# Performance work log

Hardware: AMD Instinct MI355X
Metric: run time of the kernel (lower is better)

Reference implementation:

```python
import jax, jax.numpy as jnp
import numpy as np

B, T, WN = 256, 200, 200        # batch, char_num, word_num
H, CD, WD = 512, 30, 128        # hidden_dim, char_dim, word_dim
V, K = 128, 12                  # vocab, tag_size
START, STOP = 10, 11
HH = H // 2


def lstm_dir(x_tm, m_tm, Wih, Whh, b, reverse):
    # x_tm: [T,B,I], m_tm: [T,B,1] validity mask. Packed-sequence semantics:
    # state only updates on valid steps, padded outputs are zero. reverse=True
    # replicates the backward direction of a packed bidirectional LSTM.
    z = jnp.zeros((x_tm.shape[1], Whh.shape[1]), x_tm.dtype)
    def cell(carry, inp):
        h, c = carry
        xt, mt = inp
        g = xt @ Wih.T + h @ Whh.T + b              # [B,4H], gates i,f,g,o
        i, f, gc, o = jnp.split(g, 4, axis=-1)
        cn = jax.nn.sigmoid(f) * c + jax.nn.sigmoid(i) * jnp.tanh(gc)
        hn = jax.nn.sigmoid(o) * jnp.tanh(cn)
        return (jnp.where(mt, hn, h), jnp.where(mt, cn, c)), jnp.where(mt, hn, 0.0)
    _, ys = jax.lax.scan(cell, (z, z), (x_tm, m_tm), reverse=reverse)
    return ys


def bilstm(x, lens, Wih_f, Whh_f, b_f, Wih_b, Whh_b, b_b):
    Tn = x.shape[1]
    m = jnp.arange(Tn)[None, :] < lens[:, None]     # [B,T]
    x_tm = jnp.swapaxes(x, 0, 1)
    m_tm = m.T[:, :, None]
    hf = lstm_dir(x_tm, m_tm, Wih_f, Whh_f, b_f, False)
    hb = lstm_dir(x_tm, m_tm, Wih_b, Whh_b, b_b, True)
    return jnp.swapaxes(jnp.concatenate([hf, hb], -1), 0, 1)  # [B,T,H]


def encode(characters, words, len_char, len_word,
           char_emb, char_Wih_f, char_Whh_f, char_b_f, char_Wih_b, char_Whh_b, char_b_b,
           char_lin_W, char_lin_b,
           word_Wih_f, word_Whh_f, word_b_f, word_Wih_b, word_Whh_b, word_b_b,
           word_lin_W, word_lin_b, lin1_W, lin1_b, lin2_W, lin2_b, tag_W, tag_b):
    sp = jax.nn.softplus
    char_vec = char_emb[characters]                                   # [B,T,CD]
    char_h = bilstm(char_vec, len_char, char_Wih_f, char_Whh_f, char_b_f,
                    char_Wih_b, char_Whh_b, char_b_b)                 # [B,T,H]
    char_map = sp(char_h @ char_lin_W.T + char_lin_b)                 # [B,T,H]
    word_h = bilstm(words, len_word, word_Wih_f, word_Whh_f, word_b_f,
                    word_Wih_b, word_Whh_b, word_b_b)                 # [B,WN,H]
    word_map = sp(word_h @ word_lin_W.T + word_lin_b)                 # [B,WN,T]
    word_map = word_map.reshape(word_map.shape[0], T, -1)             # view, NOT transpose
    x = jnp.concatenate([char_map, word_map], axis=2)                 # [B,T,712]
    x = sp(x @ lin1_W.T + lin1_b)
    x = sp(x @ lin2_W.T + lin2_b)
    return sp(x @ tag_W.T + tag_b)                                    # [B,T,K]


def crf_nll(logits, tags, lens, trans):
    Bn, Tn, Kn = logits.shape
    mask = jnp.arange(Tn)[None, :] < lens[:, None]                    # [B,T]
    # --- real path score (transitions indexed [from, to], START prepended) ---
    prev = jnp.concatenate([jnp.full((Bn, 1), START, tags.dtype), tags[:, :-1]], axis=1)
    emit = jnp.take_along_axis(logits, tags[..., None], axis=-1)[..., 0]
    step = jnp.where(mask, emit + trans[prev, tags], 0.0)
    last_tag = jnp.take_along_axis(tags, (lens - 1)[:, None], axis=1)[:, 0]
    real = step.sum(axis=1) + trans[last_tag, STOP]
    # --- forward algorithm (alpha init 0, first step includes transitions, as in source) ---
    def fwd(alpha, inp):
        lt, m = inp                                                   # [B,K], [B]
        sc = alpha[:, :, None] + lt[:, None, :] + trans[None]         # [B,prev,next]
        an = jax.nn.logsumexp(sc, axis=1)
        return jnp.where(m[:, None], an, alpha), None
    alpha0 = jnp.zeros((Bn, Kn), logits.dtype)
    alpha, _ = jax.lax.scan(fwd, alpha0, (jnp.swapaxes(logits, 0, 1), mask.T))
    total = jax.nn.logsumexp(alpha + trans[:, STOP][None, :], axis=1)
    return (jnp.sum(total) - jnp.sum(real)).reshape(1)


def setup_inputs() -> dict:
    key = jax.random.key(0)
    ks = jax.random.split(key, 32)
    rn = lambda k, s: jax.random.normal(k, s, jnp.float32) * 0.1
    inp = {
        "characters": jax.random.randint(ks[0], (B, T), 0, V),
        "words": jax.random.normal(ks[1], (B, WN, WD), jnp.float32),
        "tags": jax.random.randint(ks[2], (B, T), 0, K - 2),
        "len_char": jax.random.randint(ks[3], (B,), 50, T + 1),
        "len_word": jax.random.randint(ks[4], (B,), 50, WN + 1),
        "char_emb": rn(ks[5], (V, CD)),
        "char_Wih_f": rn(ks[6], (4 * HH, CD)), "char_Whh_f": rn(ks[7], (4 * HH, HH)), "char_b_f": rn(ks[8], (4 * HH,)),
        "char_Wih_b": rn(ks[9], (4 * HH, CD)), "char_Whh_b": rn(ks[10], (4 * HH, HH)), "char_b_b": rn(ks[11], (4 * HH,)),
        "char_lin_W": rn(ks[12], (H, H)), "char_lin_b": rn(ks[13], (H,)),
        "word_Wih_f": rn(ks[14], (4 * HH, WD)), "word_Whh_f": rn(ks[15], (4 * HH, HH)), "word_b_f": rn(ks[16], (4 * HH,)),
        "word_Wih_b": rn(ks[17], (4 * HH, WD)), "word_Whh_b": rn(ks[18], (4 * HH, HH)), "word_b_b": rn(ks[19], (4 * HH,)),
        "word_lin_W": rn(ks[20], (T, H)), "word_lin_b": rn(ks[21], (T,)),
        "lin1_W": rn(ks[22], (512, H + WN)), "lin1_b": rn(ks[23], (512,)),
        "lin2_W": rn(ks[24], (256, 512)), "lin2_b": rn(ks[25], (256,)),
        "tag_W": rn(ks[26], (K, 256)), "tag_b": rn(ks[27], (K,)),
    }
    trans = jax.random.normal(ks[28], (K, K), jnp.float32)
    trans = trans.at[START, :].set(-10000.0).at[:, STOP].set(-10000.0)
    inp["transitions"] = trans
    return inp


def reference(characters, words, tags, len_char, len_word,
              char_emb, char_Wih_f, char_Whh_f, char_b_f, char_Wih_b, char_Whh_b, char_b_b,
              char_lin_W, char_lin_b,
              word_Wih_f, word_Whh_f, word_b_f, word_Wih_b, word_Whh_b, word_b_b,
              word_lin_W, word_lin_b, lin1_W, lin1_b, lin2_W, lin2_b, tag_W, tag_b, transitions):
    logits = encode(characters, words, len_char, len_word,
                    char_emb, char_Wih_f, char_Whh_f, char_b_f, char_Wih_b, char_Whh_b, char_b_b,
                    char_lin_W, char_lin_b,
                    word_Wih_f, word_Whh_f, word_b_f, word_Wih_b, word_Whh_b, word_b_b,
                    word_lin_W, word_lin_b, lin1_W, lin1_b, lin2_W, lin2_b, tag_W, tag_b)
    return crf_nll(logits, tags, len_char, transitions)
```

## Files before the change

### kernel.cpp

```cpp
#include <hip/hip_runtime.h>
#include <cstdint>

typedef __attribute__((ext_vector_type(8))) short short8;
typedef __attribute__((ext_vector_type(4))) float f32x4;
typedef __attribute__((ext_vector_type(2))) float f32x2;
typedef __attribute__((ext_vector_type(4))) int i32x4;
typedef unsigned short us16;
typedef unsigned char u8;

#define DEV __device__ __forceinline__

DEV u8 f2fp8(float f){
  int p = __builtin_amdgcn_cvt_pk_fp8_f32(f, f, 0, false);
  return (u8)(p & 0xFF);
}
template<int SEL> DEV float fp8tof(int dw){
#if __has_builtin(__builtin_amdgcn_cvt_f32_fp8)
  return __builtin_amdgcn_cvt_f32_fp8(dw, SEL);
#else
  int b = (dw >> (8*SEL)) & 255;
  int e = (b>>3)&15, m = b&7;
  float v;
  if (e){ union{unsigned u; float f;} x; x.u = (unsigned)(((e+120)<<23) | (m<<20)); v = x.f; }
  else v = (float)m * 0.001953125f;
  return (b & 128) ? -v : v;
#endif
}
DEV f32x4 dq8x4(int dw){
#if __has_builtin(__builtin_amdgcn_cvt_pk_f32_fp8)
  f32x2 lo = __builtin_amdgcn_cvt_pk_f32_fp8(dw, false);
  f32x2 hi = __builtin_amdgcn_cvt_pk_f32_fp8(dw, true);
  return (f32x4){lo.x, lo.y, hi.x, hi.y};
#else
  return (f32x4){fp8tof<0>(dw), fp8tof<1>(dw), fp8tof<2>(dw), fp8tof<3>(dw)};
#endif
}
DEV float fsig(float x){
  float e = __builtin_amdgcn_exp2f(-1.4426950408889634f * x);
  return __builtin_amdgcn_rcpf(1.0f + e);
}
DEV float ftanh(float x){
  float e = __builtin_amdgcn_exp2f(-2.8853900817779268f * x);
  return fmaf(2.0f, __builtin_amdgcn_rcpf(1.0f + e), -1.0f);
}
DEV float fsoftplus(float x){
  float ax = fabsf(x);
  float e = __builtin_amdgcn_exp2f(-1.4426950408889634f * ax);
  float l = 0.69314718055994531f * __builtin_amdgcn_logf(1.0f + e);
  return fmaxf(x, 0.0f) + l;
}
DEV f32x4 mfma16f8(long a, long b, f32x4 c){
  return __builtin_amdgcn_mfma_f32_16x16x32_fp8_fp8(a, b, c, 0, 0, 0);
}
DEV unsigned pk4fp8(float a, float b, float c, float d){
  unsigned lo = (unsigned)__builtin_amdgcn_cvt_pk_fp8_f32(a, b, 0, false) & 0xFFFFu;
  unsigned hi = (unsigned)__builtin_amdgcn_cvt_pk_fp8_f32(c, d, 0, false) & 0xFFFFu;
  return lo | (hi << 16);
}

DEV void lds_barrier(){
  asm volatile("s_waitcnt lgkmcnt(0)" ::: "memory");
  __builtin_amdgcn_s_barrier();
  asm volatile("" ::: "memory");
}



DEV void swz_lstm16_one(int tid, const float* __restrict__ W, u8* __restrict__ dst){
  int e = tid & 511, chunk = tid >> 9;
  int L = e >> 3, j = e & 7;
  int kc = chunk & 7, gt = (chunk >> 3) & 3, w = chunk >> 5;
  int g = gt * 256 + w * 16 + (L & 15);
  int k = kc * 32 + (L >> 4) * 8 + j;
  dst[tid] = f2fp8(W[g * 256 + k]);
}

DEV void ctab_one(int vd, int gcol, const float* __restrict__ emb,
                  const float* __restrict__ Wih, const float* __restrict__ bb,
                  u8* __restrict__ ctab){
  int v = vd & 127, dir = vd >> 7;
  float val[4];
  #pragma unroll
  for (int gt = 0; gt < 4; ++gt){
    int g = gt * 256 + gcol;
    float s = bb[g];
    for (int k = 0; k < 30; ++k) s += emb[v * 30 + k] * Wih[g * 30 + k];
    val[gt] = s;
  }
  unsigned pk = pk4fp8(val[0], val[1], val[2], val[3]);
  *(unsigned*)&ctab[((dir * 128 + v) * 256 + gcol) * 4] = pk;
}

DEV void swz_gin_one(int tid, const float* __restrict__ W, u8* __restrict__ dst){
  int e = tid & 511, chunk = tid >> 9;
  int L = e >> 3, j = e & 7;
  int kc = chunk & 3, ntile = chunk >> 2;
  int g = ntile * 16 + (L & 15);
  int k = kc * 32 + (L >> 4) * 8 + j;
  dst[tid] = f2fp8(W[g * 128 + k]);
}

DEV void swz_ffB_one(int tid, const float* W, int N, int Kd, int KCs, u8* dst){
  int e = tid & 511, chunk = tid >> 9;
  int L = e >> 3, j = e & 7;
  int kc = chunk % KCs; int nt = chunk / KCs;
  int g = nt * 16 + (L & 15);
  int k = kc * 32 + (L >> 4) * 8 + j;
  float v = (g < N && k < Kd) ? W[g * Kd + k] : 0.0f;
  dst[tid] = f2fp8(v);
}

DEV void swz_ffA_one(int tid, const float* W, int Kd, int KCs, u8* dst){
  int e = tid & 511, chunk = tid >> 9;
  int L = e >> 3, j = e & 7;
  int kc = chunk % KCs; int mt = chunk / KCs;
  int m = mt * 16 + (L & 15);
  int k = kc * 32 + (L >> 4) * 8 + j;
  float v = (k < Kd) ? W[m * Kd + k] : 0.0f;
  dst[tid] = f2fp8(v);
}

__global__ __launch_bounds__(256) void k_pre(
    const float* __restrict__ words, u8* __restrict__ words_f8,
    const float* __restrict__ WhhA, u8* dA, const float* __restrict__ WhhB, u8* dB,
    const float* __restrict__ WhhC, u8* dC, const float* __restrict__ WhhD, u8* dD,
    const float* __restrict__ emb,
    const float* __restrict__ cWihF, const float* __restrict__ cbF,
    const float* __restrict__ cWihB, const float* __restrict__ cbB,
    u8* __restrict__ ctab,
    const float* __restrict__ gWf, const float* __restrict__ gWb,
    u8* __restrict__ dgf, u8* __restrict__ dgb,
    const float* __restrict__ W1, u8* d1, const float* __restrict__ W2, u8* d2,
    const float* __restrict__ W5, u8* d5,
    const float* __restrict__ W3, u8* d3, const float* __restrict__ W4, u8* d4)
{
  const int b = blockIdx.x, tid = threadIdx.x;
  if (b < 6400){
    int i = b * 256 + tid;
    f32x4 v = ((const f32x4*)words)[i];
    ((unsigned*)words_f8)[i] = pk4fp8(v.x, v.y, v.z, v.w);
  } else if (b < 10496){
    int bb = b - 6400;
    if (bb < 1024)       swz_lstm16_one(bb * 256 + tid, WhhA, dA);
    else if (bb < 2048)  swz_lstm16_one((bb - 1024) * 256 + tid, WhhB, dB);
    else if (bb < 3072)  swz_lstm16_one((bb - 2048) * 256 + tid, WhhC, dC);
    else                 swz_lstm16_one((bb - 3072) * 256 + tid, WhhD, dD);
  } else if (b < 10752){
    int vd = b - 10496;
    ctab_one(vd, tid, emb, (vd >> 7) ? cWihB : cWihF, (vd >> 7) ? cbB : cbF, ctab);
  } else if (b < 11776){
    int bb = b - 10752;
    if (bb < 512) swz_gin_one(bb * 256 + tid, gWf, dgf);
    else          swz_gin_one((bb - 512) * 256 + tid, gWb, dgb);
  } else if (b < 13328){
    int bb = b - 11776;
    if (bb < 1024)      swz_ffB_one(bb * 256 + tid, W1, 512, 512, 16, d1);
    else if (bb < 1536) swz_ffB_one((bb - 1024) * 256 + tid, W2, 200, 512, 16, d2);
    else                swz_ffB_one((bb - 1536) * 256 + tid, W5, 12, 256, 8, d5);
  } else {
    int bb = b - 13328;
    if (bb < 1536) swz_ffA_one(bb * 256 + tid, W3, 712, 24, d3);
    else           swz_ffA_one((bb - 1536) * 256 + tid, W4, 512, 16, d4);
  }
}

__global__ __launch_bounds__(512) void k_gin(
    const u8* __restrict__ words_f8, const u8* __restrict__ wswg_f,
    const u8* __restrict__ wswg_b, const float* __restrict__ bias_f,
    const float* __restrict__ bias_b, u8* __restrict__ gin)
{
  const int blk = blockIdx.x;
  const int d = blk / 800, rem = blk - d * 800;
  const int slice = rem / 50, tq = rem - slice * 50;
  const u8* Wsw = d ? wswg_b : wswg_f;
  const float* bias = d ? bias_b : bias_f;
  __shared__ u8 xs[16 * 136];
  __shared__ u8 sbuf[4 * 4096];
  const int tid = threadIdx.x;
  const int wv = tid >> 6, L = tid & 63;
  const int lrow = L & 15, lq = L >> 4;
  const long* WswV = (const long*)Wsw;

  long wr[8][4];
  #pragma unroll
  for (int nt = 0; nt < 8; ++nt)
    #pragma unroll
    for (int kc = 0; kc < 4; ++kc)
      wr[nt][kc] = WswV[((wv * 8 + nt) * 4 + kc) * 64 + L];
  float bv[8];
  #pragma unroll
  for (int nt = 0; nt < 8; ++nt) bv[nt] = bias[wv * 128 + nt * 16 + lrow];

  for (int i = 0; i < 4; ++i){
    const int t = tq * 4 + i;
    if (tid < 256){
      int r = tid >> 4, c8 = (tid & 15) * 8;
      *(long*)&xs[r * 136 + c8] =
        *(const long*)&words_f8[((long)(slice * 16 + r) * 200 + t) * 128 + c8];
    }
    __syncthreads();
    f32x4 acc[8];
    #pragma unroll
    for (int nt = 0; nt < 8; ++nt) acc[nt] = (f32x4){bv[nt], bv[nt], bv[nt], bv[nt]};
    #pragma unroll
    for (int kc = 0; kc < 4; ++kc){
      long af = *(const long*)&xs[lrow * 136 + kc * 32 + lq * 8];
      #pragma unroll
      for (int nt = 0; nt < 8; ++nt)
        acc[nt] = mfma16f8(af, wr[nt][kc], acc[nt]);
    }
    #pragma unroll
    for (int nt = 0; nt < 8; ++nt){
      int c = wv * 128 + nt * 16 + lrow;
      int gt = c >> 8, hcol = c & 255;
      int base = (hcol >> 4) * 256 + (hcol & 15) * 4 + gt;
      #pragma unroll
      for (int r = 0; r < 4; ++r)
        sbuf[lq * 4096 + base + r * 64] = f2fp8(acc[nt][r]);
    }
    __syncthreads();
    #pragma unroll
    for (int q = 0; q < 4; ++q){
      long ob = ((long)((d * 64 + slice * 4 + q) * 200 + t)) * 4096 + tid * 8;
      *(long*)&gin[ob] = *(const long*)&sbuf[q * 4096 + tid * 8];
    }
    __syncthreads();
  }
}

template<bool CHARV>
DEV void lstm16_body(u8* abuf, u8* cidxs,
                     const u8* __restrict__ gsrc,
                     const int* __restrict__ chars,
                     const u8* __restrict__ Wsw,
                     const int* __restrict__ lens,
                     u8* __restrict__ hout,
                     int b0, int hcol0, bool rev, long ginBase)
{
  const int tid = threadIdx.x;
  const int w = tid >> 6, L = tid & 63;
  const int lrow = L & 15, lq = L >> 4;
  const int gcol = w * 16 + lrow;
  const long* WswV = (const long*)Wsw;

  long wr[4][8];
  #pragma unroll
  for (int gt = 0; gt < 4; ++gt)
    #pragma unroll
    for (int kc = 0; kc < 8; ++kc)
      wr[gt][kc] = WswV[(((w * 4 + gt) * 8) + kc) * 64 + L];

  const int mylen = lens[b0 + lq];
  const long hbase = (long)(b0 + lq) * 200 * 512 + hcol0 + gcol;

  float cst = 0.0f;
  u8 hst = 0, houtv = 0;

  for (int e = tid; e < 1120; e += 1024) ((long*)abuf)[e] = 0;

  if constexpr (CHARV){
    if (tid < 800) cidxs[tid] = (u8)chars[(b0 + tid / 200) * 200 + tid % 200];
  }
  __syncthreads();

  const int t0 = rev ? 199 : 0;
  unsigned gw;
  if constexpr (!CHARV)
    gw = *(const unsigned*)(gsrc + (ginBase + t0) * 4096 + tid * 4);
  else
    gw = *(const unsigned*)&gsrc[((int)cidxs[lq * 200 + t0] * 256 + gcol) * 4];

  for (int tau = 0; tau < 200; ++tau){
    const int t = rev ? (199 - tau) : tau;
    u8* cur = abuf + (tau & 1) * 4480;
    u8* nxt = abuf + ((tau & 1) ^ 1) * 4480;

    f32x4 q = dq8x4((int)gw);
    f32x4 acc[4];
    #pragma unroll
    for (int gt = 0; gt < 4; ++gt)
      acc[gt] = (f32x4){q[gt], q[gt], q[gt], q[gt]};

    {
      const int tn = (tau < 199) ? (rev ? t - 1 : t + 1) : t;
      if constexpr (!CHARV)
        gw = *(const unsigned*)(gsrc + (ginBase + tn) * 4096 + tid * 4);
      else
        gw = *(const unsigned*)&gsrc[((int)cidxs[lq * 200 + tn] * 256 + gcol) * 4];
    }

    #pragma unroll
    for (int kc = 0; kc < 8; ++kc){
      long af = *(const long*)&cur[lrow * 280 + kc * 32 + lq * 8];
      #pragma unroll
      for (int gt = 0; gt < 4; ++gt)
        acc[gt] = mfma16f8(af, wr[gt][kc], acc[gt]);
    }

    const bool mk = t < mylen;
    float gi = acc[0][0], gf = acc[1][0];
    float gg = acc[2][0], go = acc[3][0];
    float cn = fsig(gf) * cst + fsig(gi) * ftanh(gg);
    if (mk) cst = cn;
    float hn = fsig(go) * ftanh(cn);
    u8 p8 = f2fp8(hn);
    if (mk) hst = p8;
    houtv = mk ? p8 : (u8)0;
    nxt[(lq * 4) * 280 + gcol] = hst;
    hout[hbase + (long)t * 512] = houtv;

    lds_barrier();
  }
}

__global__ __launch_bounds__(1024) void k_lstm(
    const int* __restrict__ characters, const u8* __restrict__ gin,
    const u8* __restrict__ ctab,
    const u8* __restrict__ wsw_cf, const u8* __restrict__ wsw_cb,
    const u8* __restrict__ wsw_wf, const u8* __restrict__ wsw_wb,
    const int* __restrict__ len_char, const int* __restrict__ len_word,
    u8* __restrict__ h_char, u8* __restrict__ h_word)
{
  const int dir    = blockIdx.x >> 6;
  const int slice4 = blockIdx.x & 63;
  const int b0 = slice4 * 4;
  __shared__ __align__(16) u8 abuf[2 * 16 * 280];
  __shared__ u8 cidxs[4 * 200];

  if (dir == 0)
    lstm16_body<true>(abuf, cidxs, ctab, characters, wsw_cf,
                      len_char, h_char, b0, 0, false, 0);
  else if (dir == 1)
    lstm16_body<true>(abuf, cidxs, ctab + 131072, characters, wsw_cb,
                      len_char, h_char, b0, 256, true, 0);
  else if (dir == 2)
    lstm16_body<false>(abuf, cidxs, gin, nullptr, wsw_wf,
                       len_word, h_word, b0, 0, false, (long)slice4 * 200);
  else
    lstm16_body<false>(abuf, cidxs, gin, nullptr, wsw_wb,
                       len_word, h_word, b0, 256, true, (long)(64 + slice4) * 200);
}

DEV void g12_body(const u8* __restrict__ A, const u8* __restrict__ Wsw,
                  const float* __restrict__ bias, int N,
                  u8* __restrict__ outp, int ocol0, int m0base, int ntbase, u8* lds)
{
  const int tid = threadIdx.x;
  const int w = tid >> 6, L = tid & 63;
  const int lrow = L & 15, lq = L >> 4;
  const long* WswV = (const long*)Wsw;
  f32x4 acc[8][2] = {};
  const int srow = tid >> 1, scol = (tid & 1) * 32;

  i32x4 v0 = *(const i32x4*)&A[(long)(m0base + srow) * 512 + scol];
  i32x4 v1 = *(const i32x4*)&A[(long)(m0base + srow) * 512 + scol + 16];

  for (int kc2 = 0; kc2 < 8; ++kc2){
    *(long*)&lds[srow * 72 + scol]      = ((const long*)&v0)[0];
    *(long*)&lds[srow * 72 + scol + 8]  = ((const long*)&v0)[1];
    *(long*)&lds[srow * 72 + scol + 16] = ((const long*)&v1)[0];
    *(long*)&lds[srow * 72 + scol + 24] = ((const long*)&v1)[1];
    lds_barrier();
    if (kc2 < 7){
      const long ab = (long)(m0base + srow) * 512 + (kc2 + 1) * 64 + scol;
      v0 = *(const i32x4*)&A[ab];
      v1 = *(const i32x4*)&A[ab + 16];
    }
    long af[2][2];
    #pragma unroll
    for (int m0 = 0; m0 < 2; ++m0)
      #pragma unroll
      for (int kk = 0; kk < 2; ++kk)
        af[m0][kk] = *(const long*)&lds[(w * 32 + m0 * 16 + lrow) * 72 + kk * 32 + lq * 8];
    #pragma unroll
    for (int kk = 0; kk < 2; ++kk)
      #pragma unroll
      for (int nt = 0; nt < 8; ++nt){
        long bf = WswV[((ntbase + nt) * 16 + kc2 * 2 + kk) * 64 + L];
        acc[nt][0] = mfma16f8(af[0][kk], bf, acc[nt][0]);
        acc[nt][1] = mfma16f8(af[1][kk], bf, acc[nt][1]);
      }
    lds_barrier();
  }
  #pragma unroll
  for (int nt = 0; nt < 8; ++nt){
    const int col = (ntbase + nt) * 16 + lrow;
    const bool valid = col < N;
    const float bvv = valid ? bias[col] : 0.0f;
    #pragma unroll
    for (int m0 = 0; m0 < 2; ++m0){
      #pragma unroll
      for (int r = 0; r < 4; ++r){
        float v = fsoftplus(acc[nt][m0][r] + bvv);
        const long row = m0base + w * 32 + m0 * 16 + lq * 4 + r;
        outp[row * 768 + ocol0 + col] = valid ? f2fp8(v) : (u8)0;
      }
    }
  }
}

__global__ __launch_bounds__(256) void k_g12(
    const u8* __restrict__ hc, const u8* __restrict__ hw,
    const u8* __restrict__ w1, const u8* __restrict__ w2,
    const float* __restrict__ b1, const float* __restrict__ b2,
    u8* __restrict__ xcat)
{
  __shared__ __align__(16) u8 lds[128 * 72];
  const int y = blockIdx.y;
  if (y < 4)
    g12_body(hc, w1, b1, 512, xcat,   0, blockIdx.x * 128, y * 8, lds);
  else
    g12_body(hw, w2, b2, 200, xcat, 512, blockIdx.x * 128, (y - 4) * 8, lds);
}

__global__ __launch_bounds__(256, 2) void k_tail(
    const u8* __restrict__ xcat, const u8* __restrict__ w3A,
    const u8* __restrict__ w4A, const u8* __restrict__ w5B,
    const float* __restrict__ b3, const float* __restrict__ b4,
    const float* __restrict__ b5, float* __restrict__ logits)
{
  __shared__ __align__(16) u8 sA[64 * 72];
  __shared__ __align__(16) u8 x1s[64 * 520];
  __shared__ __align__(16) u8 x2s[64 * 264];
  const int tid = threadIdx.x;
  const int w = tid >> 6, L = tid & 63;
  const int lrow = L & 15, lq = L >> 4;
  const int m0 = blockIdx.x * 64;
  const long* W3 = (const long*)w3A;
  const long* W4 = (const long*)w4A;
  const long* W5 = (const long*)w5B;

  f32x4 acc[8][4];
  #pragma unroll
  for (int mt = 0; mt < 8; ++mt)
    #pragma unroll
    for (int nt = 0; nt < 4; ++nt) acc[mt][nt] = (f32x4){0,0,0,0};
  const int srow = tid >> 2, sc = (tid & 3) * 16;

  i32x4 v = *(const i32x4*)&xcat[(long)(m0 + srow) * 768 + sc];
  for (int kc2 = 0; kc2 < 12; ++kc2){
    *(long*)&sA[srow * 72 + sc]     = ((const long*)&v)[0];
    *(long*)&sA[srow * 72 + sc + 8] = ((const long*)&v)[1];
    lds_barrier();
    if (kc2 < 11)
      v = *(const i32x4*)&xcat[(long)(m0 + srow) * 768 + (kc2 + 1) * 64 + sc];
    #pragma unroll
    for (int kk = 0; kk < 2; ++kk){
      long bf[4];
      #pragma unroll
      for (int nt = 0; nt < 4; ++nt)
        bf[nt] = *(const long*)&sA[(nt * 16 + lrow) * 72 + kk * 32 + lq * 8];
      #pragma unroll
      for (int mt = 0; mt < 8; ++mt){
        long af = W3[((w * 8 + mt) * 24 + kc2 * 2 + kk) * 64 + L];
        #pragma unroll
        for (int nt = 0; nt < 4; ++nt)
          acc[mt][nt] = mfma16f8(af, bf[nt], acc[mt][nt]);
      }
    }
    lds_barrier();
  }
  #pragma unroll
  for (int mt = 0; mt < 8; ++mt){
    const int ch0 = (w * 8 + mt) * 16 + lq * 4;
    f32x4 bb = *(const f32x4*)&b3[ch0];
    #pragma unroll
    for (int nt = 0; nt < 4; ++nt){
      const int bat = nt * 16 + lrow;
      unsigned pk = pk4fp8(fsoftplus(acc[mt][nt][0] + bb[0]),
                           fsoftplus(acc[mt][nt][1] + bb[1]),
                           fsoftplus(acc[mt][nt][2] + bb[2]),
                           fsoftplus(acc[mt][nt][3] + bb[3]));
      *(unsigned*)&x1s[bat * 520 + ch0] = pk;
    }
  }
  lds_barrier();

  f32x4 a2[4][4];
  #pragma unroll
  for (int mt = 0; mt < 4; ++mt)
    #pragma unroll
    for (int nt = 0; nt < 4; ++nt) a2[mt][nt] = (f32x4){0,0,0,0};
  for (int kc = 0; kc < 16; ++kc){
    long bf[4];
    #pragma unroll
    for (int nt = 0; nt < 4; ++nt)
      bf[nt] = *(const long*)&x1s[(nt * 16 + lrow) * 520 + kc * 32 + lq * 8];
    #pragma unroll
    for (int mt = 0; mt < 4; ++mt){
      long af = W4[((w * 4 + mt) * 16 + kc) * 64 + L];
      #pragma unroll
      for (int nt = 0; nt < 4; ++nt)
        a2[mt][nt] = mfma16f8(af, bf[nt], a2[mt][nt]);
    }
  }
  #pragma unroll
  for (int mt = 0; mt < 4; ++mt){
    const int ch0 = (w * 4 + mt) * 16 + lq * 4;
    f32x4 bb = *(const f32x4*)&b4[ch0];
    #pragma unroll
    for (int nt = 0; nt < 4; ++nt){
      const int bat = nt * 16 + lrow;
      unsigned pk = pk4fp8(fsoftplus(a2[mt][nt][0] + bb[0]),
                           fsoftplus(a2[mt][nt][1] + bb[1]),
                           fsoftplus(a2[mt][nt][2] + bb[2]),
                           fsoftplus(a2[mt][nt][3] + bb[3]));
      *(unsigned*)&x2s[bat * 264 + ch0] = pk;
    }
  }
  lds_barrier();

  f32x4 a3 = (f32x4){0,0,0,0};
  #pragma unroll
  for (int kc = 0; kc < 8; ++kc){
    long af = *(const long*)&x2s[(w * 16 + lrow) * 264 + kc * 32 + lq * 8];
    long bf = W5[kc * 64 + L];
    a3 = mfma16f8(af, bf, a3);
  }
  if (lrow < 12){
    float bb = b5[lrow];
    #pragma unroll
    for (int r = 0; r < 4; ++r)
      logits[(long)(m0 + w * 16 + lq * 4 + r) * 12 + lrow] = fsoftplus(a3[r] + bb);
  }
}

__global__ void k_crf(const float* __restrict__ logits, const int* __restrict__ tags,
                      const int* __restrict__ lens, const float* __restrict__ trans,
                      float* __restrict__ nll)
{
  const int b = blockIdx.x;
  const int lane = threadIdx.x;
  __shared__ float sl[2400];
  __shared__ float alpha[12];
  __shared__ float tmp[12];
  for (int e = lane; e < 2400; e += 64) sl[e] = logits[(long)b * 2400 + e];
  float tcol[12];
  if (lane < 12){
    #pragma unroll
    for (int i = 0; i < 12; ++i) tcol[i] = trans[i * 12 + lane];
    alpha[lane] = 0.0f;
  }
  const int len = lens[b];
  __syncthreads();
  for (int t = 0; t < len; ++t){
    float an = 0.0f;
    if (lane < 12){
      float mx = -3.0e38f;
      #pragma unroll
      for (int i = 0; i < 12; ++i) mx = fmaxf(mx, alpha[i] + tcol[i]);
      float ss = 0.0f;
      #pragma unroll
      for (int i = 0; i < 12; ++i)
        ss += __builtin_amdgcn_exp2f(1.4426950408889634f * (alpha[i] + tcol[i] - mx));
      an = sl[t * 12 + lane] + mx + 0.69314718055994531f * __builtin_amdgcn_logf(ss);
    }
    __syncthreads();
    if (lane < 12) alpha[lane] = an;
    __syncthreads();
  }
  if (lane < 12) tmp[lane] = alpha[lane] + trans[lane * 12 + 11];
  __syncthreads();
  float rs = 0.0f;
  for (int t = lane; t < len; t += 64){
    int tg = tags[b * 200 + t];
    int pv = (t == 0) ? 10 : tags[b * 200 + t - 1];
    rs += sl[t * 12 + tg] + trans[pv * 12 + tg];
  }
  #pragma unroll
  for (int off = 32; off > 0; off >>= 1) rs += __shfl_down(rs, off, 64);
  if (lane == 0){
    float mx = -3.0e38f;
    for (int i = 0; i < 12; ++i) mx = fmaxf(mx, tmp[i]);
    float ss = 0.0f;
    for (int i = 0; i < 12; ++i)
      ss += __builtin_amdgcn_exp2f(1.4426950408889634f * (tmp[i] - mx));
    float total = mx + 0.69314718055994531f * __builtin_amdgcn_logf(ss);
    rs += trans[tags[b * 200 + len - 1] * 12 + 11];
    nll[b] = total - rs;
  }
}

__global__ void k_sum(const float* __restrict__ nll, float* __restrict__ out){
  __shared__ float red[256];
  int t = threadIdx.x;
  red[t] = nll[t];
  __syncthreads();
  for (int s = 128; s > 0; s >>= 1){
    if (t < s) red[t] += red[t + s];
    __syncthreads();
  }
  if (t == 0) out[0] = red[0];
}

extern "C" void kernel_launch(void* const* d_in, const int* in_sizes, int n_in,
                              void* d_out, int out_size, void* d_ws, size_t ws_size,
                              hipStream_t stream)
{
  (void)in_sizes; (void)n_in; (void)out_size; (void)ws_size;
  const int*   characters = (const int*)  d_in[0];
  const float* words      = (const float*)d_in[1];
  const int*   tags       = (const int*)  d_in[2];
  const int*   len_char   = (const int*)  d_in[3];
  const int*   len_word   = (const int*)  d_in[4];
  const float* char_emb   = (const float*)d_in[5];
  const float* char_Wih_f = (const float*)d_in[6];
  const float* char_Whh_f = (const float*)d_in[7];
  const float* char_b_f   = (const float*)d_in[8];
  const float* char_Wih_b = (const float*)d_in[9];
  const float* char_Whh_b = (const float*)d_in[10];
  const float* char_b_b   = (const float*)d_in[11];
  const float* char_lin_W = (const float*)d_in[12];
  const float* char_lin_b = (const float*)d_in[13];
  const float* word_Wih_f = (const float*)d_in[14];
  const float* word_Whh_f = (const float*)d_in[15];
  const float* word_b_f   = (const float*)d_in[16];
  const float* word_Wih_b = (const float*)d_in[17];
  const float* word_Whh_b = (const float*)d_in[18];
  const float* word_b_b   = (const float*)d_in[19];
  const float* word_lin_W = (const float*)d_in[20];
  const float* word_lin_b = (const float*)d_in[21];
  const float* lin1_W     = (const float*)d_in[22];
  const float* lin1_b     = (const float*)d_in[23];
  const float* lin2_W     = (const float*)d_in[24];
  const float* lin2_b     = (const float*)d_in[25];
  const float* tag_W      = (const float*)d_in[26];
  const float* tag_b      = (const float*)d_in[27];
  const float* trans      = (const float*)d_in[28];

  char* ws = (char*)d_ws;
  size_t off = 0;
  auto take = [&](size_t bytes) -> char* {
    char* p = ws + off;
    off = (off + bytes + 511) & ~(size_t)511;
    return p;
  };
  u8*   words_f8 = (u8*)take((size_t)256*200*128);
  u8*   wsw_cf   = (u8*)take((size_t)262144);
  u8*   wsw_cb   = (u8*)take((size_t)262144);
  u8*   wsw_wf   = (u8*)take((size_t)262144);
  u8*   wsw_wb   = (u8*)take((size_t)262144);
  u8*   ctab     = (u8*)take((size_t)262144);
  u8*   wswgin_f = (u8*)take((size_t)64*4*512);
  u8*   wswgin_b = (u8*)take((size_t)64*4*512);
  u8*   wswg1    = (u8*)take((size_t)32*16*512);
  u8*   wswg2    = (u8*)take((size_t)16*16*512);
  u8*   wswg3    = (u8*)take((size_t)32*24*512);
  u8*   wswg4    = (u8*)take((size_t)16*16*512);
  u8*   wswg5    = (u8*)take((size_t)1*8*512);
  float* logits  = (float*)take((size_t)51200*12*4);
  float* nll     = (float*)take((size_t)256*4);
  u8*   h_char   = (u8*)take((size_t)51200*512);
  u8*   h_word   = (u8*)take((size_t)51200*512);
  u8*   gin      = (u8*)take((size_t)105*1024*1024);
  u8*   x_cat    = gin;

  k_pre<<<15376, 256, 0, stream>>>(
      words, words_f8,
      char_Whh_f, wsw_cf, char_Whh_b, wsw_cb, word_Whh_f, wsw_wf, word_Whh_b, wsw_wb,
      char_emb, char_Wih_f, char_b_f, char_Wih_b, char_b_b, ctab,
      word_Wih_f, word_Wih_b, wswgin_f, wswgin_b,
      char_lin_W, wswg1, word_lin_W, wswg2, tag_W, wswg5,
      lin1_W, wswg3, lin2_W, wswg4);

  k_gin<<<1600, 512, 0, stream>>>(words_f8, wswgin_f, wswgin_b, word_b_f, word_b_b, gin);

  k_lstm<<<256, 1024, 0, stream>>>(characters, gin, ctab,
                                   wsw_cf, wsw_cb, wsw_wf, wsw_wb,
                                   len_char, len_word, h_char, h_word);

  k_g12<<<dim3(400, 6), 256, 0, stream>>>(h_char, h_word, wswg1, wswg2,
                                          char_lin_b, word_lin_b, x_cat);
  k_tail<<<800, 256, 0, stream>>>(x_cat, wswg3, wswg4, wswg5,
                                  lin1_b, lin2_b, tag_b, logits);

  k_crf<<<256, 64, 0, stream>>>(logits, tags, len_char, trans, nll);
  k_sum<<<1, 256, 0, stream>>>(nll, (float*)d_out);
}
```

Measured before the change: 654.0 us.

## Fuse char/word projection GEMMs into tail MLP kernel, dropping x_cat round trip

Merges the k_g12 projection kernel into the tail kernel. Each 64-row block loads h_char (then h_word) into LDS and computes 64-column chunks of the softplus projections on the fly. Each chunk is fed directly as a K-slice of the lin1 GEMM, so the 768-wide x_cat intermediate is never written to or read from global memory and one launch is removed. In exchange, the projection weights are re-read by each of the 800 blocks and there are extra barriers per chunk.

Measured after the change: 674.2 us. +3.1%, slower.

```diff
diff --git a/kernel.cpp b/kernel.cpp
--- a/kernel.cpp
+++ b/kernel.cpp
@@ -341,109 +341,86 @@
                        len_word, h_word, b0, 256, true, (long)(64 + slice4) * 200);
 }
 
-DEV void g12_body(const u8* __restrict__ A, const u8* __restrict__ Wsw,
-                  const float* __restrict__ bias, int N,
-                  u8* __restrict__ outp, int ocol0, int m0base, int ntbase, u8* lds)
-{
-  const int tid = threadIdx.x;
-  const int w = tid >> 6, L = tid & 63;
-  const int lrow = L & 15, lq = L >> 4;
-  const long* WswV = (const long*)Wsw;
-  f32x4 acc[8][2] = {};
-  const int srow = tid >> 1, scol = (tid & 1) * 32;
-
-  i32x4 v0 = *(const i32x4*)&A[(long)(m0base + srow) * 512 + scol];
-  i32x4 v1 = *(const i32x4*)&A[(long)(m0base + srow) * 512 + scol + 16];
-
-  for (int kc2 = 0; kc2 < 8; ++kc2){
-    *(long*)&lds[srow * 72 + scol]      = ((const long*)&v0)[0];
-    *(long*)&lds[srow * 72 + scol + 8]  = ((const long*)&v0)[1];
-    *(long*)&lds[srow * 72 + scol + 16] = ((const long*)&v1)[0];
-    *(long*)&lds[srow * 72 + scol + 24] = ((const long*)&v1)[1];
-    lds_barrier();
-    if (kc2 < 7){
-      const long ab = (long)(m0base + srow) * 512 + (kc2 + 1) * 64 + scol;
-      v0 = *(const i32x4*)&A[ab];
-      v1 = *(const i32x4*)&A[ab + 16];
-    }
-    long af[2][2];
-    #pragma unroll
-    for (int m0 = 0; m0 < 2; ++m0)
-      #pragma unroll
-      for (int kk = 0; kk < 2; ++kk)
-        af[m0][kk] = *(const long*)&lds[(w * 32 + m0 * 16 + lrow) * 72 + kk * 32 + lq * 8];
-    #pragma unroll
-    for (int kk = 0; kk < 2; ++kk)
-      #pragma unroll
-      for (int nt = 0; nt < 8; ++nt){
-        long bf = WswV[((ntbase + nt) * 16 + kc2 * 2 + kk) * 64 + L];
-        acc[nt][0] = mfma16f8(af[0][kk], bf, acc[nt][0]);
-        acc[nt][1] = mfma16f8(af[1][kk], bf, acc[nt][1]);
-      }
-    lds_barrier();
-  }
-  #pragma unroll
-  for (int nt = 0; nt < 8; ++nt){
-    const int col = (ntbase + nt) * 16 + lrow;
-    const bool valid = col < N;
-    const float bvv = valid ? bias[col] : 0.0f;
-    #pragma unroll
-    for (int m0 = 0; m0 < 2; ++m0){
-      #pragma unroll
-      for (int r = 0; r < 4; ++r){
-        float v = fsoftplus(acc[nt][m0][r] + bvv);
-        const long row = m0base + w * 32 + m0 * 16 + lq * 4 + r;
-        outp[row * 768 + ocol0 + col] = valid ? f2fp8(v) : (u8)0;
-      }
-    }
-  }
-}
-
-__global__ __launch_bounds__(256) void k_g12(
+__global__ __launch_bounds__(256, 2) void k_ff(
     const u8* __restrict__ hc, const u8* __restrict__ hw,
-    const u8* __restrict__ w1, const u8* __restrict__ w2,
+    const u8* __restrict__ w1B, const u8* __restrict__ w2B,
     const float* __restrict__ b1, const float* __restrict__ b2,
-    u8* __restrict__ xcat)
-{
-  __shared__ __align__(16) u8 lds[128 * 72];
-  const int y = blockIdx.y;
-  if (y < 4)
-    g12_body(hc, w1, b1, 512, xcat,   0, blockIdx.x * 128, y * 8, lds);
-  else
-    g12_body(hw, w2, b2, 200, xcat, 512, blockIdx.x * 128, (y - 4) * 8, lds);
-}
-
-__global__ __launch_bounds__(256, 2) void k_tail(
-    const u8* __restrict__ xcat, const u8* __restrict__ w3A,
-    const u8* __restrict__ w4A, const u8* __restrict__ w5B,
+    const u8* __restrict__ w3A, const u8* __restrict__ w4A,
+    const u8* __restrict__ w5B,
     const float* __restrict__ b3, const float* __restrict__ b4,
     const float* __restrict__ b5, float* __restrict__ logits)
 {
+  __shared__ __align__(16) u8 hs[64 * 520];
   __shared__ __align__(16) u8 sA[64 * 72];
-  __shared__ __align__(16) u8 x1s[64 * 520];
   __shared__ __align__(16) u8 x2s[64 * 264];
   const int tid = threadIdx.x;
   const int w = tid >> 6, L = tid & 63;
   const int lrow = L & 15, lq = L >> 4;
   const int m0 = blockIdx.x * 64;
+  const long* W1 = (const long*)w1B;
+  const long* W2 = (const long*)w2B;
   const long* W3 = (const long*)w3A;
   const long* W4 = (const long*)w4A;
   const long* W5 = (const long*)w5B;
 
+  #pragma unroll
+  for (int q = 0; q < 8; ++q){
+    int fl = q * 256 + tid;
+    int r = fl >> 5, cc = (fl & 31) * 16;
+    *(i32x4*)&hs[r * 520 + cc] = *(const i32x4*)&hc[(long)(m0 + r) * 512 + cc];
+  }
+  lds_barrier();
+
   f32x4 acc[8][4];
   #pragma unroll
   for (int mt = 0; mt < 8; ++mt)
     #pragma unroll
     for (int nt = 0; nt < 4; ++nt) acc[mt][nt] = (f32x4){0,0,0,0};
-  const int srow = tid >> 2, sc = (tid & 3) * 16;
-
-  i32x4 v = *(const i32x4*)&xcat[(long)(m0 + srow) * 768 + sc];
-  for (int kc2 = 0; kc2 < 12; ++kc2){
-    *(long*)&sA[srow * 72 + sc]     = ((const long*)&v)[0];
-    *(long*)&sA[srow * 72 + sc + 8] = ((const long*)&v)[1];
+
+  for (int c = 0; c < 12; ++c){
+    if (c == 8){
+      #pragma unroll
+      for (int q = 0; q < 8; ++q){
+        int fl = q * 256 + tid;
+        int r = fl >> 5, cc = (fl & 31) * 16;
+        *(i32x4*)&hs[r * 520 + cc] = *(const i32x4*)&hw[(long)(m0 + r) * 512 + cc];
+      }
+      lds_barrier();
+    }
+
+    {
+      const long* WB = (c < 8) ? W1 : W2;
+      const int ntb = (c < 8) ? c * 4 : (c - 8) * 4;
+      f32x4 a2c[4];
+      #pragma unroll
+      for (int nt = 0; nt < 4; ++nt){
+        float bb = 0.0f;
+        if (c < 8) bb = b1[c * 64 + nt * 16 + lrow];
+        else { int wc = (c - 8) * 64 + nt * 16 + lrow; if (wc < 200) bb = b2[wc]; }
+        a2c[nt] = (f32x4){bb, bb, bb, bb};
+      }
+      #pragma unroll
+      for (int kc = 0; kc < 16; ++kc){
+        long af = *(const long*)&hs[(w * 16 + lrow) * 520 + kc * 32 + lq * 8];
+        #pragma unroll
+        for (int nt = 0; nt < 4; ++nt){
+          long bf = WB[((ntb + nt) * 16 + kc) * 64 + L];
+          a2c[nt] = mfma16f8(af, bf, a2c[nt]);
+        }
+      }
+      #pragma unroll
+      for (int nt = 0; nt < 4; ++nt){
+        const bool valid = (c < 8) || ((c - 8) * 64 + nt * 16 + lrow < 200);
+        #pragma unroll
+        for (int r = 0; r < 4; ++r){
+          float v = fsoftplus(a2c[nt][r]);
+          sA[(w * 16 + lq * 4 + r) * 72 + nt * 16 + lrow] =
+              valid ? f2fp8(v) : (u8)0;
+        }
+      }
+    }
     lds_barrier();
-    if (kc2 < 11)
-      v = *(const i32x4*)&xcat[(long)(m0 + srow) * 768 + (kc2 + 1) * 64 + sc];
+
     #pragma unroll
     for (int kk = 0; kk < 2; ++kk){
       long bf[4];
@@ -452,7 +429,7 @@
         bf[nt] = *(const long*)&sA[(nt * 16 + lrow) * 72 + kk * 32 + lq * 8];
       #pragma unroll
       for (int mt = 0; mt < 8; ++mt){
-        long af = W3[((w * 8 + mt) * 24 + kc2 * 2 + kk) * 64 + L];
+        long af = W3[((w * 8 + mt) * 24 + c * 2 + kk) * 64 + L];
         #pragma unroll
         for (int nt = 0; nt < 4; ++nt)
           acc[mt][nt] = mfma16f8(af, bf[nt], acc[mt][nt]);
@@ -460,6 +437,7 @@
     }
     lds_barrier();
   }
+
   #pragma unroll
   for (int mt = 0; mt < 8; ++mt){
     const int ch0 = (w * 8 + mt) * 16 + lq * 4;
@@ -471,7 +449,7 @@
                            fsoftplus(acc[mt][nt][1] + bb[1]),
                            fsoftplus(acc[mt][nt][2] + bb[2]),
                            fsoftplus(acc[mt][nt][3] + bb[3]));
-      *(unsigned*)&x1s[bat * 520 + ch0] = pk;
+      *(unsigned*)&hs[bat * 520 + ch0] = pk;
     }
   }
   lds_barrier();
@@ -485,7 +463,7 @@
     long bf[4];
     #pragma unroll
     for (int nt = 0; nt < 4; ++nt)
-      bf[nt] = *(const long*)&x1s[(nt * 16 + lrow) * 520 + kc * 32 + lq * 8];
+      bf[nt] = *(const long*)&hs[(nt * 16 + lrow) * 520 + kc * 32 + lq * 8];
     #pragma unroll
     for (int mt = 0; mt < 4; ++mt){
       long af = W4[((w * 4 + mt) * 16 + kc) * 64 + L];
@@ -653,7 +631,6 @@
   u8*   h_char   = (u8*)take((size_t)51200*512);
   u8*   h_word   = (u8*)take((size_t)51200*512);
   u8*   gin      = (u8*)take((size_t)105*1024*1024);
-  u8*   x_cat    = gin;
 
   k_pre<<<15376, 256, 0, stream>>>(
       words, words_f8,
@@ -669,10 +646,10 @@
                                    wsw_cf, wsw_cb, wsw_wf, wsw_wb,
                                    len_char, len_word, h_char, h_word);
 
-  k_g12<<<dim3(400, 6), 256, 0, stream>>>(h_char, h_word, wswg1, wswg2,
-                                          char_lin_b, word_lin_b, x_cat);
-  k_tail<<<800, 256, 0, stream>>>(x_cat, wswg3, wswg4, wswg5,
-                                  lin1_b, lin2_b, tag_b, logits);
+  k_ff<<<800, 256, 0, stream>>>(h_char, h_word, wswg1, wswg2,
+                                char_lin_b, word_lin_b,
+                                wswg3, wswg4, wswg5,
+                                lin1_b, lin2_b, tag_b, logits);
 
   k_crf<<<256, 64, 0, stream>>>(logits, tags, len_char, trans, nll);
   k_sum<<<1, 256, 0, stream>>>(nll, (float*)d_out);
```

## Fuse word input projection into recurrent LSTM kernel, drop gin buffer

Applied to the files above, without the earlier changes.

Removes the separate k_gin kernel that precomputed word-LSTM input gates into a large FP8 buffer. The word LSTM directions now load the fp8 word embeddings for the next step into a double-buffered LDS tile and compute x@Wih with extra MFMAs inside the recurrent loop, with bias initialised in registers. This removes a kernel launch and heavy global writes and reads of the gate buffer, but adds MFMA work and register pressure to the latency-bound serial recurrence. The A-operand uses only 4 real rows (lrow>>2), so three quarters of the MFMA rows are redundant.

New measurement: 968.0 us. 48.0% more time.

```diff
diff --git a/kernel.cpp b/kernel.cpp
--- a/kernel.cpp
+++ b/kernel.cpp
@@ -164,78 +164,17 @@
   }
 }
 
-__global__ __launch_bounds__(512) void k_gin(
-    const u8* __restrict__ words_f8, const u8* __restrict__ wswg_f,
-    const u8* __restrict__ wswg_b, const float* __restrict__ bias_f,
-    const float* __restrict__ bias_b, u8* __restrict__ gin)
-{
-  const int blk = blockIdx.x;
-  const int d = blk / 800, rem = blk - d * 800;
-  const int slice = rem / 50, tq = rem - slice * 50;
-  const u8* Wsw = d ? wswg_b : wswg_f;
-  const float* bias = d ? bias_b : bias_f;
-  __shared__ u8 xs[16 * 136];
-  __shared__ u8 sbuf[4 * 4096];
-  const int tid = threadIdx.x;
-  const int wv = tid >> 6, L = tid & 63;
-  const int lrow = L & 15, lq = L >> 4;
-  const long* WswV = (const long*)Wsw;
-
-  long wr[8][4];
-  #pragma unroll
-  for (int nt = 0; nt < 8; ++nt)
-    #pragma unroll
-    for (int kc = 0; kc < 4; ++kc)
-      wr[nt][kc] = WswV[((wv * 8 + nt) * 4 + kc) * 64 + L];
-  float bv[8];
-  #pragma unroll
-  for (int nt = 0; nt < 8; ++nt) bv[nt] = bias[wv * 128 + nt * 16 + lrow];
-
-  for (int i = 0; i < 4; ++i){
-    const int t = tq * 4 + i;
-    if (tid < 256){
-      int r = tid >> 4, c8 = (tid & 15) * 8;
-      *(long*)&xs[r * 136 + c8] =
-        *(const long*)&words_f8[((long)(slice * 16 + r) * 200 + t) * 128 + c8];
-    }
-    __syncthreads();
-    f32x4 acc[8];
-    #pragma unroll
-    for (int nt = 0; nt < 8; ++nt) acc[nt] = (f32x4){bv[nt], bv[nt], bv[nt], bv[nt]};
-    #pragma unroll
-    for (int kc = 0; kc < 4; ++kc){
-      long af = *(const long*)&xs[lrow * 136 + kc * 32 + lq * 8];
-      #pragma unroll
-      for (int nt = 0; nt < 8; ++nt)
-        acc[nt] = mfma16f8(af, wr[nt][kc], acc[nt]);
-    }
-    #pragma unroll
-    for (int nt = 0; nt < 8; ++nt){
-      int c = wv * 128 + nt * 16 + lrow;
-      int gt = c >> 8, hcol = c & 255;
-      int base = (hcol >> 4) * 256 + (hcol & 15) * 4 + gt;
-      #pragma unroll
-      for (int r = 0; r < 4; ++r)
-        sbuf[lq * 4096 + base + r * 64] = f2fp8(acc[nt][r]);
-    }
-    __syncthreads();
-    #pragma unroll
-    for (int q = 0; q < 4; ++q){
-      long ob = ((long)((d * 64 + slice * 4 + q) * 200 + t)) * 4096 + tid * 8;
-      *(long*)&gin[ob] = *(const long*)&sbuf[q * 4096 + tid * 8];
-    }
-    __syncthreads();
-  }
-}
-
 template<bool CHARV>
-DEV void lstm16_body(u8* abuf, u8* cidxs,
+DEV void lstm16_body(u8* abuf, u8* xbuf, u8* cidxs,
                      const u8* __restrict__ gsrc,
+                     const u8* __restrict__ xsrc,
+                     const u8* __restrict__ wswx,
+                     const float* __restrict__ bias,
                      const int* __restrict__ chars,
                      const u8* __restrict__ Wsw,
                      const int* __restrict__ lens,
                      u8* __restrict__ hout,
-                     int b0, int hcol0, bool rev, long ginBase)
+                     int b0, int hcol0, bool rev)
 {
   const int tid = threadIdx.x;
   const int w = tid >> 6, L = tid & 63;
@@ -250,6 +189,19 @@
     for (int kc = 0; kc < 8; ++kc)
       wr[gt][kc] = WswV[(((w * 4 + gt) * 8) + kc) * 64 + L];
 
+  long wrx[4][4];
+  float bv[4];
+  if constexpr (!CHARV){
+    const long* WxV = (const long*)wswx;
+    #pragma unroll
+    for (int gt = 0; gt < 4; ++gt){
+      #pragma unroll
+      for (int kc = 0; kc < 4; ++kc)
+        wrx[gt][kc] = WxV[((gt * 16 + w) * 4 + kc) * 64 + L];
+      bv[gt] = bias[gt * 256 + gcol];
+    }
+  }
+
   const int mylen = lens[b0 + lq];
   const long hbase = (long)(b0 + lq) * 200 * 512 + hcol0 + gcol;
 
@@ -261,32 +213,57 @@
   if constexpr (CHARV){
     if (tid < 800) cidxs[tid] = (u8)chars[(b0 + tid / 200) * 200 + tid % 200];
   }
+
+  const int t0 = rev ? 199 : 0;
+  unsigned gw = 0;
+  if constexpr (!CHARV){
+    if (tid < 64){
+      int r = tid >> 4, c8 = (tid & 15) * 8;
+      *(long*)&xbuf[r * 128 + c8] =
+        *(const long*)&xsrc[((long)(b0 + r) * 200 + t0) * 128 + c8];
+    }
+  }
   __syncthreads();
-
-  const int t0 = rev ? 199 : 0;
-  unsigned gw;
-  if constexpr (!CHARV)
-    gw = *(const unsigned*)(gsrc + (ginBase + t0) * 4096 + tid * 4);
-  else
+  if constexpr (CHARV)
     gw = *(const unsigned*)&gsrc[((int)cidxs[lq * 200 + t0] * 256 + gcol) * 4];
 
   for (int tau = 0; tau < 200; ++tau){
     const int t = rev ? (199 - tau) : tau;
     u8* cur = abuf + (tau & 1) * 4480;
     u8* nxt = abuf + ((tau & 1) ^ 1) * 4480;
-
-    f32x4 q = dq8x4((int)gw);
+    u8* xcur = xbuf + (tau & 1) * 512;
+    u8* xnxt = xbuf + ((tau & 1) ^ 1) * 512;
+
     f32x4 acc[4];
-    #pragma unroll
-    for (int gt = 0; gt < 4; ++gt)
-      acc[gt] = (f32x4){q[gt], q[gt], q[gt], q[gt]};
-
-    {
-      const int tn = (tau < 199) ? (rev ? t - 1 : t + 1) : t;
-      if constexpr (!CHARV)
-        gw = *(const unsigned*)(gsrc + (ginBase + tn) * 4096 + tid * 4);
-      else
-        gw = *(const unsigned*)&gsrc[((int)cidxs[lq * 200 + tn] * 256 + gcol) * 4];
+    if constexpr (!CHARV){
+      #pragma unroll
+      for (int gt = 0; gt < 4; ++gt)
+        acc[gt] = (f32x4){bv[gt], bv[gt], bv[gt], bv[gt]};
+    } else {
+      f32x4 q = dq8x4((int)gw);
+      #pragma unroll
+      for (int gt = 0; gt < 4; ++gt)
+        acc[gt] = (f32x4){q[gt], q[gt], q[gt], q[gt]};
+    }
+
+    const int tn = (tau < 199) ? (rev ? t - 1 : t + 1) : t;
+    long xv = 0;
+    if constexpr (!CHARV){
+      if (tid < 64)
+        xv = *(const long*)&xsrc[((long)(b0 + (tid >> 4)) * 200 + tn) * 128 +
+                                 (tid & 15) * 8];
+    } else {
+      gw = *(const unsigned*)&gsrc[((int)cidxs[lq * 200 + tn] * 256 + gcol) * 4];
+    }
+
+    if constexpr (!CHARV){
+      #pragma unroll
+      for (int kc = 0; kc < 4; ++kc){
+        long afx = *(const long*)&xcur[(lrow >> 2) * 128 + kc * 32 + lq * 8];
+        #pragma unroll
+        for (int gt = 0; gt < 4; ++gt)
+          acc[gt] = mfma16f8(afx, wrx[gt][kc], acc[gt]);
+      }
     }
 
     #pragma unroll
@@ -309,13 +286,19 @@
     nxt[(lq * 4) * 280 + gcol] = hst;
     hout[hbase + (long)t * 512] = houtv;
 
+    if constexpr (!CHARV){
+      if (tid < 64)
+        *(long*)&xnxt[(tid >> 4) * 128 + (tid & 15) * 8] = xv;
+    }
     lds_barrier();
   }
 }
 
 __global__ __launch_bounds__(1024) void k_lstm(
-    const int* __restrict__ characters, const u8* __restrict__ gin,
+    const int* __restrict__ characters, const u8* __restrict__ words_f8,
     const u8* __restrict__ ctab,
+    const u8* __restrict__ wswx_f, const u8* __restrict__ wswx_b,
+    const float* __restrict__ wb_f, const float* __restrict__ wb_b,
     const u8* __restrict__ wsw_cf, const u8* __restrict__ wsw_cb,
     const u8* __restrict__ wsw_wf, const u8* __restrict__ wsw_wb,
     const int* __restrict__ len_char, const int* __restrict__ len_word,
@@ -325,20 +308,21 @@
   const int slice4 = blockIdx.x & 63;
   const int b0 = slice4 * 4;
   __shared__ __align__(16) u8 abuf[2 * 16 * 280];
+  __shared__ __align__(16) u8 xbuf[2 * 512];
   __shared__ u8 cidxs[4 * 200];
 
   if (dir == 0)
-    lstm16_body<true>(abuf, cidxs, ctab, characters, wsw_cf,
-                      len_char, h_char, b0, 0, false, 0);
+    lstm16_body<true>(abuf, xbuf, cidxs, ctab, nullptr, nullptr, nullptr,
+                      characters, wsw_cf, len_char, h_char, b0, 0, false);
   else if (dir == 1)
-    lstm16_body<true>(abuf, cidxs, ctab + 131072, characters, wsw_cb,
-                      len_char, h_char, b0, 256, true, 0);
+    lstm16_body<true>(abuf, xbuf, cidxs, ctab + 131072, nullptr, nullptr, nullptr,
+                      characters, wsw_cb, len_char, h_char, b0, 256, true);
   else if (dir == 2)
-    lstm16_body<false>(abuf, cidxs, gin, nullptr, wsw_wf,
-                       len_word, h_word, b0, 0, false, (long)slice4 * 200);
+    lstm16_body<false>(abuf, xbuf, cidxs, nullptr, words_f8, wswx_f, wb_f,
+                       nullptr, wsw_wf, len_word, h_word, b0, 0, false);
   else
-    lstm16_body<false>(abuf, cidxs, gin, nullptr, wsw_wb,
-                       len_word, h_word, b0, 256, true, (long)(64 + slice4) * 200);
+    lstm16_body<false>(abuf, xbuf, cidxs, nullptr, words_f8, wswx_b, wb_b,
+                       nullptr, wsw_wb, len_word, h_word, b0, 256, true);
 }
 
 DEV void g12_body(const u8* __restrict__ A, const u8* __restrict__ Wsw,
@@ -652,8 +636,7 @@
   float* nll     = (float*)take((size_t)256*4);
   u8*   h_char   = (u8*)take((size_t)51200*512);
   u8*   h_word   = (u8*)take((size_t)51200*512);
-  u8*   gin      = (u8*)take((size_t)105*1024*1024);
-  u8*   x_cat    = gin;
+  u8*   x_cat    = (u8*)take((size_t)51200*768);
 
   k_pre<<<15376, 256, 0, stream>>>(
       words, words_f8,
@@ -663,9 +646,8 @@
       char_lin_W, wswg1, word_lin_W, wswg2, tag_W, wswg5,
       lin1_W, wswg3, lin2_W, wswg4);
 
-  k_gin<<<1600, 512, 0, stream>>>(words_f8, wswgin_f, wswgin_b, word_b_f, word_b_b, gin);
-
-  k_lstm<<<256, 1024, 0, stream>>>(characters, gin, ctab,
+  k_lstm<<<256, 1024, 0, stream>>>(characters, words_f8, ctab,
+                                   wswgin_f, wswgin_b, word_b_f, word_b_b,
                                    wsw_cf, wsw_cb, wsw_wf, wsw_wb,
                                    len_char, len_word, h_char, h_word);
 
```
